# Performance work log

Measured on AMD Instinct MI355X. Metric: run time of the kernel, lower is better.

## Reference

```python
import jax, jax.numpy as jnp
import numpy as np

NUM_LAYERS = 4
HIDDEN = 64
IN_CH = 3
OUT_CH = 1


def setup_inputs() -> dict:
    key = jax.random.key(0)
    ks = jax.random.split(key, 16)
    s = 0.1  # weight init scale
    x = jax.random.normal(ks[0], (2, 64, 64, IN_CH), dtype=jnp.float32)
    lift_w = jax.random.normal(ks[1], (IN_CH, HIDDEN), dtype=jnp.float32) * s
    lift_b = jax.random.normal(ks[2], (HIDDEN,), dtype=jnp.float32) * s
    blk_w = jax.random.normal(ks[3], (NUM_LAYERS, HIDDEN, HIDDEN), dtype=jnp.float32) * s
    blk_b = jax.random.normal(ks[4], (NUM_LAYERS, HIDDEN), dtype=jnp.float32) * s
    q_w = jax.random.normal(ks[5], (NUM_LAYERS, HIDDEN, HIDDEN), dtype=jnp.float32) * s
    q_b = jax.random.normal(ks[6], (NUM_LAYERS, HIDDEN), dtype=jnp.float32) * s
    k_w = jax.random.normal(ks[7], (NUM_LAYERS, HIDDEN, HIDDEN), dtype=jnp.float32) * s
    k_b = jax.random.normal(ks[8], (NUM_LAYERS, HIDDEN), dtype=jnp.float32) * s
    v_w = jax.random.normal(ks[9], (NUM_LAYERS, HIDDEN, HIDDEN), dtype=jnp.float32) * s
    v_b = jax.random.normal(ks[10], (NUM_LAYERS, HIDDEN), dtype=jnp.float32) * s
    proj_w = jax.random.normal(ks[11], (HIDDEN, OUT_CH), dtype=jnp.float32) * s
    proj_b = jax.random.normal(ks[12], (OUT_CH,), dtype=jnp.float32) * s
    return {"x": x, "lift_w": lift_w, "lift_b": lift_b,
            "blk_w": blk_w, "blk_b": blk_b,
            "q_w": q_w, "q_b": q_b, "k_w": k_w, "k_b": k_b,
            "v_w": v_w, "v_b": v_b, "proj_w": proj_w, "proj_b": proj_b}


def reference(x, lift_w, lift_b, blk_w, blk_b, q_w, q_b, k_w, k_b, v_w, v_b, proj_w, proj_b):
    prefix = x.shape[:-1]           # (B, H, W)
    B = x.shape[0]
    xf = x.reshape(B, -1, x.shape[-1])   # [B, N, in_ch]
    N = xf.shape[1]
    h = xf @ lift_w + lift_b             # [B, N, d]
    d = h.shape[-1]
    scale = 1.0 / jnp.sqrt(jnp.float32(d))
    for i in range(NUM_LAYERS):
        q = h @ q_w[i] + q_b[i]
        k = h @ k_w[i] + k_b[i]
        v = h @ v_w[i] + v_b[i]
        # full dense kernel, as in torch.bmm(q, k^T)/sqrt(d)
        kern = jnp.einsum('bnd,bmd->bnm', q, k) * scale     # [B, N, N]
        integral = jnp.einsum('bnm,bmd->bnd', kern, v) / N  # [B, N, d]
        wh = h @ blk_w[i] + blk_b[i]
        h = jax.nn.gelu(wh + integral, approximate=False)   # torch F.gelu default = exact erf
    out = h @ proj_w + proj_b                               # [B, N, out_ch]
    return out.reshape(*prefix, out.shape[-1])
```

## Files before the change

kernel.cpp:

```cpp
#include <hip/hip_runtime.h>
#include <hip/hip_bf16.h>
#include <math.h>


#define NLAYER 4
#define NB 2
#define NN 4096
#define DD 64
#define RPB 32
#define NT 256
#define NBLK 256
#define SHP 68
#define C0F (1.0f/32768.0f)
#define PSZ 2304
#define NCH 128
#define CHW 18

typedef __hip_bfloat16 bf16;
typedef unsigned long long u64t;

#define O_SH   0
#define O_B1   2176
#define O_B2   6528
#define O_B3   10880
#define O_B4   15232
#define O_B5   19584
#define O_SS   23936
#define O_SU   24000
#define O_BK   24064
#define O_BQ   24128
#define O_BV   24192
#define O_BE   24256
#define O_QK   24320
#define O_KQ   24384
#define O_QBK  24448
#define O_RED  24512
#define SM_TOT 24768

__device__ __forceinline__ float b2f(const bf16 v) { return __bfloat162float(v); }
__device__ __forceinline__ float bfu(unsigned s) {
    return __uint_as_float(s << 16);
}

template <typename T> struct Acc;
template <> struct Acc<float> {
    static __device__ __forceinline__ float ld(const void* p, int i) { return ((const float*)p)[i]; }
    static __device__ __forceinline__ void st(void* p, int i, float v) { ((float*)p)[i] = v; }
};
template <> struct Acc<bf16> {
    static __device__ __forceinline__ float ld(const void* p, int i) { return b2f(((const bf16*)p)[i]); }
    static __device__ __forceinline__ void st(void* p, int i, float v) { ((bf16*)p)[i] = __float2bfloat16(v); }
};

__device__ __forceinline__ float gelu_exact(float x) {
    return 0.5f * x * (1.0f + erff(x * 0.70710678118654752f));
}

__device__ __forceinline__ float2 ldc2(const float* p) {
    u64t v = __hip_atomic_load((const u64t*)p, __ATOMIC_RELAXED, __HIP_MEMORY_SCOPE_AGENT);
    float2 r;
    r.x = __uint_as_float((unsigned)v);
    r.y = __uint_as_float((unsigned)(v >> 32));
    return r;
}
__device__ __forceinline__ void stc2(float* p, float a, float b) {
    u64t v = ((u64t)__float_as_uint(b) << 32) | (u64t)__float_as_uint(a);
    __hip_atomic_store((u64t*)p, v, __ATOMIC_RELAXED, __HIP_MEMORY_SCOPE_AGENT);
}
__device__ __forceinline__ unsigned ldw(unsigned* p) {
    return __hip_atomic_load(p, __ATOMIC_RELAXED, __HIP_MEMORY_SCOPE_AGENT);
}
__device__ __forceinline__ void stw(unsigned* p, unsigned v) {
    __hip_atomic_store(p, v, __ATOMIC_RELAXED, __HIP_MEMORY_SCOPE_AGENT);
}
__device__ __forceinline__ void pollw(unsigned* p, unsigned ep) {
    int guard = 0;
    while (ldw(p) < ep && ++guard < (1 << 18)) __builtin_amdgcn_s_sleep(2);
}

__device__ __forceinline__ void mm4x4(float (&acc)[4][4],
    float4 L0, float4 L1, float4 L2, float4 L3,
    float4 R0, float4 R1, float4 R2, float4 R3)
{
    const float L[4][4] = {{L0.x,L0.y,L0.z,L0.w},{L1.x,L1.y,L1.z,L1.w},
                           {L2.x,L2.y,L2.z,L2.w},{L3.x,L3.y,L3.z,L3.w}};
    const float R[4][4] = {{R0.x,R0.y,R0.z,R0.w},{R1.x,R1.y,R1.z,R1.w},
                           {R2.x,R2.y,R2.z,R2.w},{R3.x,R3.y,R3.z,R3.w}};
    #pragma unroll
    for (int a = 0; a < 4; a++)
        #pragma unroll
        for (int k = 0; k < 4; k++)
            #pragma unroll
            for (int b = 0; b < 4; b++)
                acc[a][b] += L[a][k] * R[k][b];
}

__device__ __forceinline__ void outer4x4(float (&acc)[4][4], float4 A, float4 B)
{
    const float Aa[4] = {A.x, A.y, A.z, A.w};
    const float Ba[4] = {B.x, B.y, B.z, B.w};
    #pragma unroll
    for (int a = 0; a < 4; a++)
        #pragma unroll
        for (int b = 0; b < 4; b++)
            acc[a][b] += Aa[a] * Ba[b];
}

template <typename T>
__device__ void run_net(
    const void* x, const void* lw, const void* lb,
    const void* blkw, const void* blkb,
    const void* qw, const void* qb, const void* kw, const void* kb,
    const void* vw, const void* vb, const void* pw, const void* pb,
    void* out, float* Gpart, float* Gg,
    unsigned* aflag, unsigned* cflag,
    float* smem, int blk, int t)
{
    float (*sH)[SHP] = (float(*)[SHP])(smem + O_SH);
    float (*W1)[SHP] = (float(*)[SHP])(smem + O_B1);
    float (*W2)[SHP] = (float(*)[SHP])(smem + O_B2);
    float (*B3)[SHP] = (float(*)[SHP])(smem + O_B3);
    float (*W4)[SHP] = (float(*)[SHP])(smem + O_B4);
    float (*W5)[SHP] = (float(*)[SHP])(smem + O_B5);
    float* PS  = smem + O_B3;
    float* RED = smem + O_B3;
    float* sS  = smem + O_SS;
    float* suS = smem + O_SU;
    float* bkS = smem + O_BK;
    float* bqS = smem + O_BQ;
    float* bvS = smem + O_BV;
    float* beS = smem + O_BE;
    float* qkS = smem + O_QK;
    float* kqS = smem + O_KQ;
    float* qbkS = smem + O_QBK;
    float (*red)[DD] = (float(*)[DD])(smem + O_RED);

    const int row0 = blk * RPB;
    const int bb = blk >> 7;
    const int r = t >> 4, c4 = (t & 15) << 2;
    const int i4 = t >> 4, j4 = t & 15;
    const int r0 = i4 << 2, c0 = j4 << 2;
    const int Ltr = t & 63, gtr = t >> 6;

    #pragma unroll
    for (int a = 0; a < 2; a++) {
        const int row = r + 16 * a, gr = row0 + row;
        float x0 = Acc<T>::ld(x, gr * 3 + 0);
        float x1 = Acc<T>::ld(x, gr * 3 + 1);
        float x2 = Acc<T>::ld(x, gr * 3 + 2);
        float o[4];
        #pragma unroll
        for (int b = 0; b < 4; b++) {
            int c = c4 + b;
            o[b] = Acc<T>::ld(lb, c) + x0 * Acc<T>::ld(lw, c)
                 + x1 * Acc<T>::ld(lw, DD + c) + x2 * Acc<T>::ld(lw, 2 * DD + c);
        }
        *(float4*)&sH[row][c4] = make_float4(o[0], o[1], o[2], o[3]);
    }
    __syncthreads();

    float4 pAf[4], pBf[4];
    unsigned pq[8], pk[8];

    for (int layer = 0; layer < NLAYER; layer++) {
        const unsigned ep = (unsigned)(layer + 1);
        float* GgL = Gg + (size_t)(layer * NB + bb) * PSZ;
        const int wOff = layer * DD * DD, bOff = layer * DD;

        if constexpr (sizeof(T) == 4) {
            const float* qwf = (const float*)qw + wOff;
            const float* kwf = (const float*)kw + wOff;
            #pragma unroll
            for (int k = 0; k < 4; k++) {
                pAf[k] = *(const float4*)(qwf + 4 * (k * NT + t));
                pBf[k] = *(const float4*)(kwf + 4 * (k * NT + t));
            }
        } else {
            const unsigned* q32 = (const unsigned*)qw + (wOff >> 1);
            const unsigned* k32 = (const unsigned*)kw + (wOff >> 1);
            #pragma unroll
            for (int k = 0; k < 8; k++) {
                pq[k] = q32[t + k * NT];
                pk[k] = k32[t + k * NT];
            }
        }

        {
            if (i4 <= j4) {
                float m[4][4];
                #pragma unroll
                for (int a = 0; a < 4; a++)
                    #pragma unroll
                    for (int b = 0; b < 4; b++) m[a][b] = 0.f;
                #pragma unroll 8
                for (int n = 0; n < RPB; n++)
                    outer4x4(m, *(const float4*)&sH[n][r0], *(const float4*)&sH[n][c0]);
                float* dst = PS + (i4 * (33 - i4) / 2 + (j4 - i4)) * 16;
                #pragma unroll
                for (int a = 0; a < 4; a++)
                    #pragma unroll
                    for (int b = 0; b < 4; b++) dst[a * 4 + b] = m[a][b];
            }
            if (t < DD) {
                float ss = 0.f;
                #pragma unroll 8
                for (int n = 0; n < RPB; n++) ss += sH[n][t];
                PS[2176 + t] = ss;
                PS[2240 + t] = 0.f;
            }
        }
        __syncthreads();
        {
            float* slot = Gpart + (size_t)blk * PSZ;
            #pragma unroll
            for (int k2 = 0; k2 < 4; k2++) {
                const int idx = 2 * (t + k2 * NT);
                stc2(&slot[idx], PS[idx], PS[idx + 1]);
            }
            if (t < 128) {
                const int idx = 2 * (t + 4 * NT);
                stc2(&slot[idx], PS[idx], PS[idx + 1]);
            }
        }
        __syncthreads();
        if (t == 0) stw(&aflag[blk], ep);

        if constexpr (sizeof(T) == 4) {
            #pragma unroll
            for (int k = 0; k < 4; k++) {
                const int i2 = 4 * (k * NT + t);
                *(float4*)&W1[i2 >> 6][i2 & 63] = pAf[k];
                *(float4*)&W4[i2 >> 6][i2 & 63] = pBf[k];
            }
        } else {
            #pragma unroll
            for (int k = 0; k < 8; k++) {
                const int i2 = 2 * (t + k * NT);
                unsigned uq = pq[k], uk = pk[k];
                *(float2*)&W1[i2 >> 6][i2 & 63] = make_float2(bfu(uq & 0xffffu), bfu(uq >> 16));
                *(float2*)&W4[i2 >> 6][i2 & 63] = make_float2(bfu(uk & 0xffffu), bfu(uk >> 16));
            }
        }
        if (t < DD) {
            bkS[t] = Acc<T>::ld(kb, bOff + t);
            bqS[t] = Acc<T>::ld(qb, bOff + t);
            bvS[t] = Acc<T>::ld(vb, bOff + t);
        }
        __syncthreads();

        #pragma unroll
        for (int k = 0; k < 16; k++) {
            const int i = (Ltr + gtr + 4 * k) & 63;
            W5[i][Ltr] = W4[Ltr][i];
        }
        __syncthreads();

        {
            float acc[4][4];
            #pragma unroll
            for (int a = 0; a < 4; a++)
                #pragma unroll
                for (int b = 0; b < 4; b++) acc[a][b] = 0.f;
            #pragma unroll 2
            for (int e = 0; e < DD; e += 4)
                mm4x4(acc,
                      *(const float4*)&W1[r0 + 0][e], *(const float4*)&W1[r0 + 1][e],
                      *(const float4*)&W1[r0 + 2][e], *(const float4*)&W1[r0 + 3][e],
                      *(const float4*)&W5[e + 0][c0], *(const float4*)&W5[e + 1][c0],
                      *(const float4*)&W5[e + 2][c0], *(const float4*)&W5[e + 3][c0]);
            #pragma unroll
            for (int a = 0; a < 4; a++)
                *(float4*)&W2[r0 + a][c0] = make_float4(acc[a][0], acc[a][1], acc[a][2], acc[a][3]);

            if (t < DD) {
                float u = 0.f;
                for (int e = 0; e < DD; e++) u += W1[t][e] * bkS[e];
                qkS[t] = u;
            } else if (t < 2 * DD) {
                const int rr = t - DD;
                float u = 0.f;
                for (int e = 0; e < DD; e++) u += W4[rr][e] * bqS[e];
                kqS[rr] = u;
            } else if (t == 2 * DD) {
                float u = 0.f;
                for (int e = 0; e < DD; e++) u += bqS[e] * bkS[e];
                qbkS[0] = u;
            }
        }
        __syncthreads();

        if constexpr (sizeof(T) == 4) {
            const float* vwf = (const float*)vw + wOff;
            const float* bwf = (const float*)blkw + wOff;
            #pragma unroll
            for (int k = 0; k < 4; k++) {
                pAf[k] = *(const float4*)(vwf + 4 * (k * NT + t));
                pBf[k] = *(const float4*)(bwf + 4 * (k * NT + t));
            }
        } else {
            const unsigned* v32 = (const unsigned*)vw + (wOff >> 1);
            const unsigned* b32 = (const unsigned*)blkw + (wOff >> 1);
            #pragma unroll
            for (int k = 0; k < 8; k++) {
                pq[k] = v32[t + k * NT];
                pk[k] = b32[t + k * NT];
            }
        }

        {
            if (t < NCH) pollw(&aflag[bb * NCH + t], ep);
            __syncthreads();
            const int chunk = blk & (NCH - 1);
            if (t < 144) {
                const int g = t / 9, p2 = t % 9;
                const float* base = Gpart + (size_t)(bb * NCH + g * 8) * PSZ
                                  + chunk * CHW + 2 * p2;
                float ax = 0.f, ay = 0.f;
                #pragma unroll
                for (int s2 = 0; s2 < 8; s2++) {
                    float2 v = ldc2(base + (size_t)s2 * PSZ);
                    ax += v.x; ay += v.y;
                }
                RED[g * 20 + 2 * p2]     = ax;
                RED[g * 20 + 2 * p2 + 1] = ay;
            }
            __syncthreads();
            if (t < 9) {
                float s0 = 0.f, s1 = 0.f;
                #pragma unroll
                for (int g = 0; g < 16; g++) {
                    s0 += RED[g * 20 + 2 * t];
                    s1 += RED[g * 20 + 2 * t + 1];
                }
                stc2(&GgL[chunk * CHW + 2 * t], s0, s1);
            }
            __syncthreads();
            if (t == 0) stw(&cflag[blk], ep);
        }

        if constexpr (sizeof(T) == 4) {
            #pragma unroll
            for (int k = 0; k < 4; k++) {
                const int i2 = 4 * (k * NT + t);
                *(float4*)&W1[i2 >> 6][i2 & 63] = pAf[k];
                *(float4*)&W4[i2 >> 6][i2 & 63] = pBf[k];
            }
        } else {
            #pragma unroll
            for (int k = 0; k < 8; k++) {
                const int i2 = 2 * (t + k * NT);
                unsigned uv = pq[k], ub = pk[k];
                *(float2*)&W1[i2 >> 6][i2 & 63] = make_float2(bfu(uv & 0xffffu), bfu(uv >> 16));
                *(float2*)&W4[i2 >> 6][i2 & 63] = make_float2(bfu(ub & 0xffffu), bfu(ub >> 16));
            }
        }

        {
            if (t < NCH) pollw(&cflag[bb * NCH + t], ep);
            __syncthreads();
            if (i4 <= j4) {
                const float* src = GgL + (i4 * (33 - i4) / 2 + (j4 - i4)) * 16;
                #pragma unroll
                for (int a = 0; a < 4; a++)
                    *(float4*)&B3[r0 + a][c0] = *(const float4*)&src[a * 4];
            } else {
                const float* src = GgL + (j4 * (33 - j4) / 2 + (i4 - j4)) * 16;
                #pragma unroll
                for (int a = 0; a < 4; a++)
                    #pragma unroll
                    for (int b = 0; b < 4; b++)
                        B3[r0 + a][c0 + b] = src[b * 4 + a];
            }
            if (t < DD) sS[t] = GgL[2176 + t];
            __syncthreads();
        }

        {
            float acc[4][4];
            #pragma unroll
            for (int a = 0; a < 4; a++)
                #pragma unroll
                for (int b = 0; b < 4; b++) acc[a][b] = sS[r0 + a] * bvS[c0 + b];
            #pragma unroll 2
            for (int e = 0; e < DD; e += 4)
                mm4x4(acc,
                      *(const float4*)&B3[r0 + 0][e], *(const float4*)&B3[r0 + 1][e],
                      *(const float4*)&B3[r0 + 2][e], *(const float4*)&B3[r0 + 3][e],
                      *(const float4*)&W1[e + 0][c0], *(const float4*)&W1[e + 1][c0],
                      *(const float4*)&W1[e + 2][c0], *(const float4*)&W1[e + 3][c0]);
            #pragma unroll
            for (int a = 0; a < 4; a++)
                *(float4*)&W5[r0 + a][c0] = make_float4(acc[a][0], acc[a][1], acc[a][2], acc[a][3]);
        }
        {
            const int c = t & 63, q = t >> 6;
            float u = 0.f;
            #pragma unroll
            for (int d2 = 0; d2 < 16; d2++) u += sS[q * 16 + d2] * W1[q * 16 + d2][c];
            red[q][c] = u;
        }
        __syncthreads();
        if (t < DD) suS[t] = red[0][t] + red[1][t] + red[2][t] + red[3][t] + (float)NN * bvS[t];
        __syncthreads();

        {
            float acc[4][4];
            #pragma unroll
            for (int a = 0; a < 4; a++)
                #pragma unroll
                for (int b = 0; b < 4; b++) acc[a][b] = qkS[r0 + a] * suS[c0 + b];
            #pragma unroll 2
            for (int e = 0; e < DD; e += 4)
                mm4x4(acc,
                      *(const float4*)&W2[r0 + 0][e], *(const float4*)&W2[r0 + 1][e],
                      *(const float4*)&W2[r0 + 2][e], *(const float4*)&W2[r0 + 3][e],
                      *(const float4*)&W5[e + 0][c0], *(const float4*)&W5[e + 1][c0],
                      *(const float4*)&W5[e + 2][c0], *(const float4*)&W5[e + 3][c0]);
            float wloc[4][4];
            #pragma unroll
            for (int a = 0; a < 4; a++)
                #pragma unroll
                for (int b = 0; b < 4; b++)
                    wloc[a][b] = W4[r0 + a][c0 + b] + C0F * acc[a][b];
            {
                const int c = t & 63, q = t >> 6;
                float u = 0.f;
                #pragma unroll
                for (int e2 = 0; e2 < 16; e2++) u += kqS[q * 16 + e2] * W5[q * 16 + e2][c];
                red[q][c] = u;
            }
            __syncthreads();
            #pragma unroll
            for (int a = 0; a < 4; a++)
                *(float4*)&B3[r0 + a][c0] = make_float4(wloc[a][0], wloc[a][1], wloc[a][2], wloc[a][3]);
            if (t < DD) beS[t] = Acc<T>::ld(blkb, bOff + t)
                               + C0F * (red[0][t] + red[1][t] + red[2][t] + red[3][t]
                                        + qbkS[0] * suS[t]);
        }
        __syncthreads();

        float o[2][4];
        #pragma unroll
        for (int a = 0; a < 2; a++) {
            const int row = r + 16 * a;
            float acc2[4];
            #pragma unroll
            for (int b = 0; b < 4; b++) acc2[b] = beS[c4 + b];
            for (int d = 0; d < DD; d++) {
                float hv = sH[row][d];
                float4 w4 = *(const float4*)&B3[d][c4];
                acc2[0] += hv * w4.x; acc2[1] += hv * w4.y;
                acc2[2] += hv * w4.z; acc2[3] += hv * w4.w;
            }
            #pragma unroll
            for (int b = 0; b < 4; b++) o[a][b] = gelu_exact(acc2[b]);
        }

        if (layer == NLAYER - 1) {
            float pbv = Acc<T>::ld(pb, 0);
            #pragma unroll
            for (int a = 0; a < 2; a++) {
                float p = 0.f;
                #pragma unroll
                for (int b = 0; b < 4; b++) p += o[a][b] * Acc<T>::ld(pw, c4 + b);
                p += __shfl_xor(p, 1);
                p += __shfl_xor(p, 2);
                p += __shfl_xor(p, 4);
                p += __shfl_xor(p, 8);
                if ((t & 15) == 0) Acc<T>::st(out, row0 + r + 16 * a, p + pbv);
            }
        } else {
            __syncthreads();
            #pragma unroll
            for (int a = 0; a < 2; a++)
                *(float4*)&sH[r + 16 * a][c4] =
                    make_float4(o[a][0], o[a][1], o[a][2], o[a][3]);
            __syncthreads();
        }
    }
}

__global__ __launch_bounds__(NT, 1) void gno_kernel(
    const void* x, const void* lw, const void* lb,
    const void* blkw, const void* blkb,
    const void* qw, const void* qb, const void* kw, const void* kb,
    const void* vw, const void* vb, const void* pw, const void* pb,
    void* out, float* Gpart, float* Gg, unsigned* bar, int mode)
{
    __shared__ alignas(16) float smem[SM_TOT];
    __shared__ int stot;

    const int blk = blockIdx.x, t = threadIdx.x;

    bool isbf;
    if (mode >= 0) {
        isbf = (mode == 1);
    } else {
        if (t == 0) stot = 0;
        __syncthreads();
        int cdt = 0;
        const unsigned int* xw = (const unsigned int*)x;
        for (int i = t; i < 8192; i += NT) {
            unsigned u = xw[i] & 0xFFFFu;
            int e = (u >> 7) & 0xFF;
            cdt += (u == 0u || (e >= 100 && e <= 142)) ? 1 : 0;
        }
        atomicAdd(&stot, cdt);
        __syncthreads();
        isbf = (stot > 4915);
    }

    unsigned* aflag = bar;
    unsigned* cflag = bar + 256;

    if (isbf)
        run_net<bf16>(x, lw, lb, blkw, blkb, qw, qb, kw, kb, vw, vb, pw, pb,
                      out, Gpart, Gg, aflag, cflag, smem, blk, t);
    else
        run_net<float>(x, lw, lb, blkw, blkb, qw, qb, kw, kb, vw, vb, pw, pb,
                       out, Gpart, Gg, aflag, cflag, smem, blk, t);
}

extern "C" void kernel_launch(void* const* d_in, const int* in_sizes, int n_in,
                              void* d_out, int out_size, void* d_ws, size_t ws_size,
                              hipStream_t stream)
{
    const void* x    = d_in[0];
    const void* lw   = d_in[1];
    const void* lb   = d_in[2];
    const void* blkw = d_in[3];
    const void* blkb = d_in[4];
    const void* qw   = d_in[5];
    const void* qb   = d_in[6];
    const void* kw   = d_in[7];
    const void* kb   = d_in[8];
    const void* vw   = d_in[9];
    const void* vb   = d_in[10];
    const void* pw   = d_in[11];
    const void* pb   = d_in[12];

    int mode = -1;
    if (in_sizes && n_in > 0) {
        if (in_sizes[0] == 49152) mode = 1;
        else if (in_sizes[0] == 98304) mode = 0;
    }

    unsigned* bar = (unsigned*)d_ws;
    float* Gpart  = (float*)d_ws + 512;
    float* Gg     = Gpart + (size_t)NBLK * PSZ;

    hipMemsetAsync(bar, 0, 512 * sizeof(unsigned), stream);
    gno_kernel<<<NBLK, NT, 0, stream>>>(x, lw, lb, blkw, blkb, qw, qb, kw, kb,
                                        vw, vb, pw, pb, d_out, Gpart, Gg, bar, mode);
}
```

Measured before the change: 187.6 us.

## Double threads per block to 512 and split per-thread tiles in half

After: 323.2 us. +72.2%, slower.

```diff
diff --git a/kernel.cpp b/kernel.cpp
--- a/kernel.cpp
+++ b/kernel.cpp
@@ -8,7 +8,7 @@
 #define NN 4096
 #define DD 64
 #define RPB 32
-#define NT 256
+#define NT 512
 #define NBLK 256
 #define SHP 68
 #define C0F (1.0f/32768.0f)
@@ -25,22 +25,21 @@
 #define O_B3   10880
 #define O_B4   15232
 #define O_B5   19584
-#define O_SS   23936
-#define O_SU   24000
-#define O_BK   24064
-#define O_BQ   24128
-#define O_BV   24192
-#define O_BE   24256
-#define O_QK   24320
-#define O_KQ   24384
-#define O_QBK  24448
-#define O_RED  24512
-#define SM_TOT 24768
+#define O_PS2  23936
+#define O_SS   26240
+#define O_SU   26304
+#define O_BK   26368
+#define O_BQ   26432
+#define O_BV   26496
+#define O_BE   26560
+#define O_QK   26624
+#define O_KQ   26688
+#define O_QBK  26752
+#define O_RED  26816
+#define SM_TOT 27328
 
 __device__ __forceinline__ float b2f(const bf16 v) { return __bfloat162float(v); }
-__device__ __forceinline__ float bfu(unsigned s) {
-    return __uint_as_float(s << 16);
-}
+__device__ __forceinline__ float bfu(unsigned s) { return __uint_as_float(s << 16); }
 
 template <typename T> struct Acc;
 template <> struct Acc<float> {
@@ -78,21 +77,21 @@
     while (ldw(p) < ep && ++guard < (1 << 18)) __builtin_amdgcn_s_sleep(2);
 }
 
-__device__ __forceinline__ void mm4x4(float (&acc)[4][4],
+__device__ __forceinline__ void mm4x2(float (&acc)[4][2],
     float4 L0, float4 L1, float4 L2, float4 L3,
-    float4 R0, float4 R1, float4 R2, float4 R3)
+    float2 R0, float2 R1, float2 R2, float2 R3)
 {
     const float L[4][4] = {{L0.x,L0.y,L0.z,L0.w},{L1.x,L1.y,L1.z,L1.w},
                            {L2.x,L2.y,L2.z,L2.w},{L3.x,L3.y,L3.z,L3.w}};
-    const float R[4][4] = {{R0.x,R0.y,R0.z,R0.w},{R1.x,R1.y,R1.z,R1.w},
-                           {R2.x,R2.y,R2.z,R2.w},{R3.x,R3.y,R3.z,R3.w}};
+    const float Rx[4] = {R0.x, R1.x, R2.x, R3.x};
+    const float Ry[4] = {R0.y, R1.y, R2.y, R3.y};
     #pragma unroll
     for (int a = 0; a < 4; a++)
         #pragma unroll
-        for (int k = 0; k < 4; k++)
-            #pragma unroll
-            for (int b = 0; b < 4; b++)
-                acc[a][b] += L[a][k] * R[k][b];
+        for (int k = 0; k < 4; k++) {
+            acc[a][0] += L[a][k] * Rx[k];
+            acc[a][1] += L[a][k] * Ry[k];
+        }
 }
 
 __device__ __forceinline__ void outer4x4(float (&acc)[4][4], float4 A, float4 B)
@@ -123,6 +122,7 @@
     float (*W4)[SHP] = (float(*)[SHP])(smem + O_B4);
     float (*W5)[SHP] = (float(*)[SHP])(smem + O_B5);
     float* PS  = smem + O_B3;
+    float* PS2 = smem + O_PS2;
     float* RED = smem + O_B3;
     float* sS  = smem + O_SS;
     float* suS = smem + O_SU;
@@ -137,53 +137,33 @@
 
     const int row0 = blk * RPB;
     const int bb = blk >> 7;
-    const int r = t >> 4, c4 = (t & 15) << 2;
-    const int i4 = t >> 4, j4 = t & 15;
+    const int ar = t >> 4, ac4 = (t & 15) << 2;
+    const int half = t >> 8, tt = t & 255;
+    const int i4 = tt >> 4, j4 = tt & 15;
     const int r0 = i4 << 2, c0 = j4 << 2;
+    const int er0 = (t >> 5) << 2, ec0 = (t & 31) << 1;
     const int Ltr = t & 63, gtr = t >> 6;
 
-    #pragma unroll
-    for (int a = 0; a < 2; a++) {
-        const int row = r + 16 * a, gr = row0 + row;
+    {
+        const int gr = row0 + ar;
         float x0 = Acc<T>::ld(x, gr * 3 + 0);
         float x1 = Acc<T>::ld(x, gr * 3 + 1);
         float x2 = Acc<T>::ld(x, gr * 3 + 2);
         float o[4];
         #pragma unroll
         for (int b = 0; b < 4; b++) {
-            int c = c4 + b;
+            int c = ac4 + b;
             o[b] = Acc<T>::ld(lb, c) + x0 * Acc<T>::ld(lw, c)
                  + x1 * Acc<T>::ld(lw, DD + c) + x2 * Acc<T>::ld(lw, 2 * DD + c);
         }
-        *(float4*)&sH[row][c4] = make_float4(o[0], o[1], o[2], o[3]);
+        *(float4*)&sH[ar][ac4] = make_float4(o[0], o[1], o[2], o[3]);
     }
     __syncthreads();
-
-    float4 pAf[4], pBf[4];
-    unsigned pq[8], pk[8];
 
     for (int layer = 0; layer < NLAYER; layer++) {
         const unsigned ep = (unsigned)(layer + 1);
         float* GgL = Gg + (size_t)(layer * NB + bb) * PSZ;
         const int wOff = layer * DD * DD, bOff = layer * DD;
-
-        if constexpr (sizeof(T) == 4) {
-            const float* qwf = (const float*)qw + wOff;
-            const float* kwf = (const float*)kw + wOff;
-            #pragma unroll
-            for (int k = 0; k < 4; k++) {
-                pAf[k] = *(const float4*)(qwf + 4 * (k * NT + t));
-                pBf[k] = *(const float4*)(kwf + 4 * (k * NT + t));
-            }
-        } else {
-            const unsigned* q32 = (const unsigned*)qw + (wOff >> 1);
-            const unsigned* k32 = (const unsigned*)kw + (wOff >> 1);
-            #pragma unroll
-            for (int k = 0; k < 8; k++) {
-                pq[k] = q32[t + k * NT];
-                pk[k] = k32[t + k * NT];
-            }
-        }
 
         {
             if (i4 <= j4) {
@@ -192,53 +172,61 @@
                 for (int a = 0; a < 4; a++)
                     #pragma unroll
                     for (int b = 0; b < 4; b++) m[a][b] = 0.f;
+                const int nb = half * 16;
                 #pragma unroll 8
-                for (int n = 0; n < RPB; n++)
+                for (int n = nb; n < nb + 16; n++)
                     outer4x4(m, *(const float4*)&sH[n][r0], *(const float4*)&sH[n][c0]);
-                float* dst = PS + (i4 * (33 - i4) / 2 + (j4 - i4)) * 16;
+                float* dst = (half ? PS2 : PS) + (i4 * (33 - i4) / 2 + (j4 - i4)) * 16;
                 #pragma unroll
                 for (int a = 0; a < 4; a++)
                     #pragma unroll
                     for (int b = 0; b < 4; b++) dst[a * 4 + b] = m[a][b];
             }
-            if (t < DD) {
+            if (t < 2 * DD) {
+                const int col = t & 63, hf = t >> 6;
+                float* dst = hf ? PS2 : PS;
                 float ss = 0.f;
+                const int nb = hf * 16;
                 #pragma unroll 8
-                for (int n = 0; n < RPB; n++) ss += sH[n][t];
-                PS[2176 + t] = ss;
-                PS[2240 + t] = 0.f;
+                for (int n = nb; n < nb + 16; n++) ss += sH[n][col];
+                dst[2176 + col] = ss;
+                dst[2240 + col] = 0.f;
             }
         }
         __syncthreads();
         {
             float* slot = Gpart + (size_t)blk * PSZ;
             #pragma unroll
-            for (int k2 = 0; k2 < 4; k2++) {
+            for (int k2 = 0; k2 < 2; k2++) {
                 const int idx = 2 * (t + k2 * NT);
-                stc2(&slot[idx], PS[idx], PS[idx + 1]);
+                stc2(&slot[idx], PS[idx] + PS2[idx], PS[idx + 1] + PS2[idx + 1]);
             }
             if (t < 128) {
-                const int idx = 2 * (t + 4 * NT);
-                stc2(&slot[idx], PS[idx], PS[idx + 1]);
+                const int idx = 2 * (t + 2 * NT);
+                stc2(&slot[idx], PS[idx] + PS2[idx], PS[idx + 1] + PS2[idx + 1]);
             }
         }
         __syncthreads();
         if (t == 0) stw(&aflag[blk], ep);
 
         if constexpr (sizeof(T) == 4) {
+            const float* qwf = (const float*)qw + wOff;
+            const float* kwf = (const float*)kw + wOff;
+            #pragma unroll
+            for (int k = 0; k < 2; k++) {
+                const int i2 = 4 * (t + k * NT);
+                *(float4*)&W1[i2 >> 6][i2 & 63] = *(const float4*)(qwf + i2);
+                *(float4*)&W4[i2 >> 6][i2 & 63] = *(const float4*)(kwf + i2);
+            }
+        } else {
+            const unsigned* q32 = (const unsigned*)qw + (wOff >> 1);
+            const unsigned* k32 = (const unsigned*)kw + (wOff >> 1);
             #pragma unroll
             for (int k = 0; k < 4; k++) {
-                const int i2 = 4 * (k * NT + t);
-                *(float4*)&W1[i2 >> 6][i2 & 63] = pAf[k];
-                *(float4*)&W4[i2 >> 6][i2 & 63] = pBf[k];
-            }
-        } else {
-            #pragma unroll
-            for (int k = 0; k < 8; k++) {
-                const int i2 = 2 * (t + k * NT);
-                unsigned uq = pq[k], uk = pk[k];
-                *(float2*)&W1[i2 >> 6][i2 & 63] = make_float2(bfu(uq & 0xffffu), bfu(uq >> 16));
-                *(float2*)&W4[i2 >> 6][i2 & 63] = make_float2(bfu(uk & 0xffffu), bfu(uk >> 16));
+                const int i2 = t + k * NT;
+                unsigned uq = q32[i2], uk = k32[i2];
+                *(float2*)&W1[(2 * i2) >> 6][(2 * i2) & 63] = make_float2(bfu(uq & 0xffffu), bfu(uq >> 16));
+                *(float2*)&W4[(2 * i2) >> 6][(2 * i2) & 63] = make_float2(bfu(uk & 0xffffu), bfu(uk >> 16));
             }
         }
         if (t < DD) {
@@ -246,31 +234,59 @@
             bqS[t] = Acc<T>::ld(qb, bOff + t);
             bvS[t] = Acc<T>::ld(vb, bOff + t);
         }
-        __syncthreads();
+
+        {
+            if (t < NCH) pollw(&aflag[bb * NCH + t], ep);
+            __syncthreads();
+            const int chunk = blk & (NCH - 1);
+            if (t < 144) {
+                const int g = t / 9, p2 = t % 9;
+                const float* base = Gpart + (size_t)(bb * NCH + g * 8) * PSZ
+                                  + chunk * CHW + 2 * p2;
+                float ax = 0.f, ay = 0.f;
+                #pragma unroll
+                for (int s2 = 0; s2 < 8; s2++) {
+                    float2 v = ldc2(base + (size_t)s2 * PSZ);
+                    ax += v.x; ay += v.y;
+                }
+                RED[g * 20 + 2 * p2]     = ax;
+                RED[g * 20 + 2 * p2 + 1] = ay;
+            }
+            __syncthreads();
+            if (t < 9) {
+                float s0 = 0.f, s1 = 0.f;
+                #pragma unroll
+                for (int g = 0; g < 16; g++) {
+                    s0 += RED[g * 20 + 2 * t];
+                    s1 += RED[g * 20 + 2 * t + 1];
+                }
+                stc2(&GgL[chunk * CHW + 2 * t], s0, s1);
+            }
+            __syncthreads();
+            if (t == 0) stw(&cflag[blk], ep);
+        }
 
         #pragma unroll
-        for (int k = 0; k < 16; k++) {
-            const int i = (Ltr + gtr + 4 * k) & 63;
+        for (int k = 0; k < 8; k++) {
+            const int i = (Ltr + gtr + 8 * k) & 63;
             W5[i][Ltr] = W4[Ltr][i];
         }
         __syncthreads();
 
         {
-            float acc[4][4];
-            #pragma unroll
-            for (int a = 0; a < 4; a++)
-                #pragma unroll
-                for (int b = 0; b < 4; b++) acc[a][b] = 0.f;
+            float acc[4][2];
+            #pragma unroll
+            for (int a = 0; a < 4; a++) { acc[a][0] = 0.f; acc[a][1] = 0.f; }
             #pragma unroll 2
             for (int e = 0; e < DD; e += 4)
-                mm4x4(acc,
-                      *(const float4*)&W1[r0 + 0][e], *(const float4*)&W1[r0 + 1][e],
-                      *(const float4*)&W1[r0 + 2][e], *(const float4*)&W1[r0 + 3][e],
-                      *(const float4*)&W5[e + 0][c0], *(const float4*)&W5[e + 1][c0],
-                      *(const float4*)&W5[e + 2][c0], *(const float4*)&W5[e + 3][c0]);
+                mm4x2(acc,
+                      *(const float4*)&W1[er0 + 0][e], *(const float4*)&W1[er0 + 1][e],
+                      *(const float4*)&W1[er0 + 2][e], *(const float4*)&W1[er0 + 3][e],
+                      *(const float2*)&W5[e + 0][ec0], *(const float2*)&W5[e + 1][ec0],
+                      *(const float2*)&W5[e + 2][ec0], *(const float2*)&W5[e + 3][ec0]);
             #pragma unroll
             for (int a = 0; a < 4; a++)
-                *(float4*)&W2[r0 + a][c0] = make_float4(acc[a][0], acc[a][1], acc[a][2], acc[a][3]);
+                *(float2*)&W2[er0 + a][ec0] = make_float2(acc[a][0], acc[a][1]);
 
             if (t < DD) {
                 float u = 0.f;
@@ -293,194 +309,154 @@
             const float* vwf = (const float*)vw + wOff;
             const float* bwf = (const float*)blkw + wOff;
             #pragma unroll
-            for (int k = 0; k < 4; k++) {
-                pAf[k] = *(const float4*)(vwf + 4 * (k * NT + t));
-                pBf[k] = *(const float4*)(bwf + 4 * (k * NT + t));
+            for (int k = 0; k < 2; k++) {
+                const int i2 = 4 * (t + k * NT);
+                *(float4*)&W1[i2 >> 6][i2 & 63] = *(const float4*)(vwf + i2);
+                *(float4*)&W4[i2 >> 6][i2 & 63] = *(const float4*)(bwf + i2);
             }
         } else {
             const unsigned* v32 = (const unsigned*)vw + (wOff >> 1);
             const unsigned* b32 = (const unsigned*)blkw + (wOff >> 1);
             #pragma unroll
-            for (int k = 0; k < 8; k++) {
-                pq[k] = v32[t + k * NT];
-                pk[k] = b32[t + k * NT];
-            }
-        }
-
-        {
-            if (t < NCH) pollw(&aflag[bb * NCH + t], ep);
-            __syncthreads();
-            const int chunk = blk & (NCH - 1);
-            if (t < 144) {
-                const int g = t / 9, p2 = t % 9;
-                const float* base = Gpart + (size_t)(bb * NCH + g * 8) * PSZ
-                                  + chunk * CHW + 2 * p2;
-                float ax = 0.f, ay = 0.f;
-                #pragma unroll
-                for (int s2 = 0; s2 < 8; s2++) {
-                    float2 v = ldc2(base + (size_t)s2 * PSZ);
-                    ax += v.x; ay += v.y;
+            for (int k = 0; k < 4; k++) {
+                const int i2 = t + k * NT;
+                unsigned uv = v32[i2], ub = b32[i2];
+                *(float2*)&W1[(2 * i2) >> 6][(2 * i2) & 63] = make_float2(bfu(uv & 0xffffu), bfu(uv >> 16));
+                *(float2*)&W4[(2 * i2) >> 6][(2 * i2) & 63] = make_float2(bfu(ub & 0xffffu), bfu(ub >> 16));
+            }
+        }
+
+        {
+            if (t < NCH) pollw(&cflag[bb * NCH + t], ep);
+            __syncthreads();
+            if (t < 256) {
+                if (i4 <= j4) {
+                    const float* src = GgL + (i4 * (33 - i4) / 2 + (j4 - i4)) * 16;
+                    #pragma unroll
+                    for (int a = 0; a < 4; a++)
+                        *(float4*)&B3[r0 + a][c0] = *(const float4*)&src[a * 4];
+                } else {
+                    const float* src = GgL + (j4 * (33 - j4) / 2 + (i4 - j4)) * 16;
+                    #pragma unroll
+                    for (int a = 0; a < 4; a++)
+                        #pragma unroll
+                        for (int b = 0; b < 4; b++)
+                            B3[r0 + a][c0 + b] = src[b * 4 + a];
                 }
-                RED[g * 20 + 2 * p2]     = ax;
-                RED[g * 20 + 2 * p2 + 1] = ay;
-            }
-            __syncthreads();
-            if (t < 9) {
-                float s0 = 0.f, s1 = 0.f;
-                #pragma unroll
-                for (int g = 0; g < 16; g++) {
-                    s0 += RED[g * 20 + 2 * t];
-                    s1 += RED[g * 20 + 2 * t + 1];
-                }
-                stc2(&GgL[chunk * CHW + 2 * t], s0, s1);
-            }
-            __syncthreads();
-            if (t == 0) stw(&cflag[blk], ep);
-        }
-
-        if constexpr (sizeof(T) == 4) {
-            #pragma unroll
-            for (int k = 0; k < 4; k++) {
-                const int i2 = 4 * (k * NT + t);
-                *(float4*)&W1[i2 >> 6][i2 & 63] = pAf[k];
-                *(float4*)&W4[i2 >> 6][i2 & 63] = pBf[k];
-            }
-        } else {
-            #pragma unroll
-            for (int k = 0; k < 8; k++) {
-                const int i2 = 2 * (t + k * NT);
-                unsigned uv = pq[k], ub = pk[k];
-                *(float2*)&W1[i2 >> 6][i2 & 63] = make_float2(bfu(uv & 0xffffu), bfu(uv >> 16));
-                *(float2*)&W4[i2 >> 6][i2 & 63] = make_float2(bfu(ub & 0xffffu), bfu(ub >> 16));
-            }
-        }
-
-        {
-            if (t < NCH) pollw(&cflag[bb * NCH + t], ep);
-            __syncthreads();
-            if (i4 <= j4) {
-                const float* src = GgL + (i4 * (33 - i4) / 2 + (j4 - i4)) * 16;
-                #pragma unroll
-                for (int a = 0; a < 4; a++)
-                    *(float4*)&B3[r0 + a][c0] = *(const float4*)&src[a * 4];
-            } else {
-                const float* src = GgL + (j4 * (33 - j4) / 2 + (i4 - j4)) * 16;
-                #pragma unroll
-                for (int a = 0; a < 4; a++)
-                    #pragma unroll
-                    for (int b = 0; b < 4; b++)
-                        B3[r0 + a][c0 + b] = src[b * 4 + a];
-            }
-            if (t < DD) sS[t] = GgL[2176 + t];
-            __syncthreads();
-        }
-
-        {
-            float acc[4][4];
-            #pragma unroll
-            for (int a = 0; a < 4; a++)
-                #pragma unroll
-                for (int b = 0; b < 4; b++) acc[a][b] = sS[r0 + a] * bvS[c0 + b];
+            } else if (t < 256 + DD) {
+                sS[t - 256] = GgL[2176 + (t - 256)];
+            }
+            __syncthreads();
+        }
+
+        {
+            float acc[4][2];
+            #pragma unroll
+            for (int a = 0; a < 4; a++) {
+                acc[a][0] = sS[er0 + a] * bvS[ec0 + 0];
+                acc[a][1] = sS[er0 + a] * bvS[ec0 + 1];
+            }
             #pragma unroll 2
             for (int e = 0; e < DD; e += 4)
-                mm4x4(acc,
-                      *(const float4*)&B3[r0 + 0][e], *(const float4*)&B3[r0 + 1][e],
-                      *(const float4*)&B3[r0 + 2][e], *(const float4*)&B3[r0 + 3][e],
-                      *(const float4*)&W1[e + 0][c0], *(const float4*)&W1[e + 1][c0],
-                      *(const float4*)&W1[e + 2][c0], *(const float4*)&W1[e + 3][c0]);
+                mm4x2(acc,
+                      *(const float4*)&B3[er0 + 0][e], *(const float4*)&B3[er0 + 1][e],
+                      *(const float4*)&B3[er0 + 2][e], *(const float4*)&B3[er0 + 3][e],
+                      *(const float2*)&W1[e + 0][ec0], *(const float2*)&W1[e + 1][ec0],
+                      *(const float2*)&W1[e + 2][ec0], *(const float2*)&W1[e + 3][ec0]);
             #pragma unroll
             for (int a = 0; a < 4; a++)
-                *(float4*)&W5[r0 + a][c0] = make_float4(acc[a][0], acc[a][1], acc[a][2], acc[a][3]);
+                *(float2*)&W5[er0 + a][ec0] = make_float2(acc[a][0], acc[a][1]);
         }
         {
             const int c = t & 63, q = t >> 6;
             float u = 0.f;
             #pragma unroll
-            for (int d2 = 0; d2 < 16; d2++) u += sS[q * 16 + d2] * W1[q * 16 + d2][c];
+            for (int d2 = 0; d2 < 8; d2++) u += sS[q * 8 + d2] * W1[q * 8 + d2][c];
             red[q][c] = u;
         }
         __syncthreads();
-        if (t < DD) suS[t] = red[0][t] + red[1][t] + red[2][t] + red[3][t] + (float)NN * bvS[t];
-        __syncthreads();
-
-        {
-            float acc[4][4];
-            #pragma unroll
-            for (int a = 0; a < 4; a++)
-                #pragma unroll
-                for (int b = 0; b < 4; b++) acc[a][b] = qkS[r0 + a] * suS[c0 + b];
+        if (t < DD) {
+            float u = 0.f;
+            #pragma unroll
+            for (int g = 0; g < 8; g++) u += red[g][t];
+            suS[t] = u + (float)NN * bvS[t];
+        }
+        __syncthreads();
+
+        {
+            float acc[4][2];
+            #pragma unroll
+            for (int a = 0; a < 4; a++) {
+                acc[a][0] = qkS[er0 + a] * suS[ec0 + 0];
+                acc[a][1] = qkS[er0 + a] * suS[ec0 + 1];
+            }
             #pragma unroll 2
             for (int e = 0; e < DD; e += 4)
-                mm4x4(acc,
-                      *(const float4*)&W2[r0 + 0][e], *(const float4*)&W2[r0 + 1][e],
-                      *(const float4*)&W2[r0 + 2][e], *(const float4*)&W2[r0 + 3][e],
-                      *(const float4*)&W5[e + 0][c0], *(const float4*)&W5[e + 1][c0],
-                      *(const float4*)&W5[e + 2][c0], *(const float4*)&W5[e + 3][c0]);
-            float wloc[4][4];
-            #pragma unroll
-            for (int a = 0; a < 4; a++)
-                #pragma unroll
-                for (int b = 0; b < 4; b++)
-                    wloc[a][b] = W4[r0 + a][c0 + b] + C0F * acc[a][b];
+                mm4x2(acc,
+                      *(const float4*)&W2[er0 + 0][e], *(const float4*)&W2[er0 + 1][e],
+                      *(const float4*)&W2[er0 + 2][e], *(const float4*)&W2[er0 + 3][e],
+                      *(const float2*)&W5[e + 0][ec0], *(const float2*)&W5[e + 1][ec0],
+                      *(const float2*)&W5[e + 2][ec0], *(const float2*)&W5[e + 3][ec0]);
+            float wloc[4][2];
+            #pragma unroll
+            for (int a = 0; a < 4; a++) {
+                wloc[a][0] = W4[er0 + a][ec0 + 0] + C0F * acc[a][0];
+                wloc[a][1] = W4[er0 + a][ec0 + 1] + C0F * acc[a][1];
+            }
             {
                 const int c = t & 63, q = t >> 6;
                 float u = 0.f;
                 #pragma unroll
-                for (int e2 = 0; e2 < 16; e2++) u += kqS[q * 16 + e2] * W5[q * 16 + e2][c];
+                for (int e2 = 0; e2 < 8; e2++) u += kqS[q * 8 + e2] * W5[q * 8 + e2][c];
                 red[q][c] = u;
             }
             __syncthreads();
             #pragma unroll
             for (int a = 0; a < 4; a++)
-                *(float4*)&B3[r0 + a][c0] = make_float4(wloc[a][0], wloc[a][1], wloc[a][2], wloc[a][3]);
-            if (t < DD) beS[t] = Acc<T>::ld(blkb, bOff + t)
-                               + C0F * (red[0][t] + red[1][t] + red[2][t] + red[3][t]
-                                        + qbkS[0] * suS[t]);
-        }
-        __syncthreads();
-
-        float o[2][4];
-        #pragma unroll
-        for (int a = 0; a < 2; a++) {
-            const int row = r + 16 * a;
+                *(float2*)&B3[er0 + a][ec0] = make_float2(wloc[a][0], wloc[a][1]);
+            if (t < DD) {
+                float u = 0.f;
+                #pragma unroll
+                for (int g = 0; g < 8; g++) u += red[g][t];
+                beS[t] = Acc<T>::ld(blkb, bOff + t) + C0F * (u + qbkS[0] * suS[t]);
+            }
+        }
+        __syncthreads();
+
+        float o[4];
+        {
             float acc2[4];
             #pragma unroll
-            for (int b = 0; b < 4; b++) acc2[b] = beS[c4 + b];
+            for (int b = 0; b < 4; b++) acc2[b] = beS[ac4 + b];
             for (int d = 0; d < DD; d++) {
-                float hv = sH[row][d];
-                float4 w4 = *(const float4*)&B3[d][c4];
+                float hv = sH[ar][d];
+                float4 w4 = *(const float4*)&B3[d][ac4];
                 acc2[0] += hv * w4.x; acc2[1] += hv * w4.y;
                 acc2[2] += hv * w4.z; acc2[3] += hv * w4.w;
             }
             #pragma unroll
-            for (int b = 0; b < 4; b++) o[a][b] = gelu_exact(acc2[b]);
+            for (int b = 0; b < 4; b++) o[b] = gelu_exact(acc2[b]);
         }
 
         if (layer == NLAYER - 1) {
             float pbv = Acc<T>::ld(pb, 0);
-            #pragma unroll
-            for (int a = 0; a < 2; a++) {
-                float p = 0.f;
-                #pragma unroll
-                for (int b = 0; b < 4; b++) p += o[a][b] * Acc<T>::ld(pw, c4 + b);
-                p += __shfl_xor(p, 1);
-                p += __shfl_xor(p, 2);
-                p += __shfl_xor(p, 4);
-                p += __shfl_xor(p, 8);
-                if ((t & 15) == 0) Acc<T>::st(out, row0 + r + 16 * a, p + pbv);
-            }
+            float p = 0.f;
+            #pragma unroll
+            for (int b = 0; b < 4; b++) p += o[b] * Acc<T>::ld(pw, ac4 + b);
+            p += __shfl_xor(p, 1);
+            p += __shfl_xor(p, 2);
+            p += __shfl_xor(p, 4);
+            p += __shfl_xor(p, 8);
+            if ((t & 15) == 0) Acc<T>::st(out, row0 + ar, p + pbv);
         } else {
             __syncthreads();
-            #pragma unroll
-            for (int a = 0; a < 2; a++)
-                *(float4*)&sH[r + 16 * a][c4] =
-                    make_float4(o[a][0], o[a][1], o[a][2], o[a][3]);
+            *(float4*)&sH[ar][ac4] = make_float4(o[0], o[1], o[2], o[3]);
             __syncthreads();
         }
     }
 }
 
-__global__ __launch_bounds__(NT, 1) void gno_kernel(
+__global__ __launch_bounds__(NT, 2) void gno_kernel(
     const void* x, const void* lw, const void* lb,
     const void* blkw, const void* blkb,
     const void* qw, const void* qb, const void* kw, const void* kb,
```
